# Kernel tuning notes

Hardware: AMD Instinct MI355X
Metric: run time of the kernel (lower is better)

## Reference

```python
import jax, jax.numpy as jnp
import numpy as np

B, L, D_IN, D_EDGE, H, D = 2, 384, 256, 128, 8, 32
SCALE = D ** (-0.5)


def setup_inputs() -> dict:
    key = jax.random.key(0)
    ks = jax.random.split(key, 12)
    hd = H * D
    s_in = D_IN ** -0.5
    s_e = D_EDGE ** -0.5
    return {
        "node_feat": jax.random.normal(ks[0], (B, L, D_IN), jnp.float32),
        "edge_feat": jax.random.normal(ks[1], (B, L, L, D_EDGE), jnp.float32),
        "edge_mask": (jax.random.uniform(ks[2], (B, L, L)) > 0.15).astype(jnp.float32),
        "Wq": jax.random.normal(ks[3], (D_IN, hd), jnp.float32) * s_in,
        "bq": jnp.zeros((hd,), jnp.float32),
        "Wk": jax.random.normal(ks[4], (D_IN, hd), jnp.float32) * s_in,
        "bk": jnp.zeros((hd,), jnp.float32),
        "Wv": jax.random.normal(ks[5], (D_IN, hd), jnp.float32) * s_in,
        "bv": jnp.zeros((hd,), jnp.float32),
        "We": jax.random.normal(ks[6], (D_EDGE, hd), jnp.float32) * s_e,
        "Wu": jax.random.normal(ks[7], (D_IN, hd), jnp.float32) * s_in,
        "bu": jnp.zeros((hd,), jnp.float32),
    }


def _split_heads(t):
    # (b, l, h*d) -> (b, h, l, d)
    b, l, _ = t.shape
    return t.reshape(b, l, H, D).transpose(0, 2, 1, 3)


def reference(node_feat, edge_feat, edge_mask, Wq, bq, Wk, bk, Wv, bv, We, Wu, bu):
    q = _split_heads(node_feat @ Wq + bq)
    k = _split_heads(node_feat @ Wk + bk)
    v = _split_heads(node_feat @ Wv + bv)
    # edge embedding: (b, i, j, h*d) -> (b, h, i, j, d)
    b, l = edge_feat.shape[0], edge_feat.shape[1]
    e = (edge_feat @ We).reshape(b, l, l, H, D).transpose(0, 3, 1, 2, 4)
    logit = jnp.einsum('bhid,bhjd->bhij', q, k)
    logit = logit + jnp.einsum('bhid,bhijd->bhij', q, e)
    att = logit * SCALE
    att = att + ((1.0 - edge_mask) * -1e9)[:, None, :, :]
    att = jax.nn.softmax(att, axis=-1)  # dropout is identity in eval / p=0
    updated = jnp.einsum('bhij,bhjd->bhid', att, v)
    updated = updated + jnp.einsum('bhij,bhijd->bhid', att, e)
    updated = updated.transpose(0, 2, 1, 3).reshape(b, l, H * D)
    return (node_feat @ Wu + bu) + updated
```

## Files before the change

### kernel.cpp

```cpp
#include <hip/hip_runtime.h>
#include <cstdint>

#define NB 2
#define LL 384
#define DIN 256
#define DE 128
#define NH 8
#define DH 32
#define HD 256
#define SCALE 0.17677669529663687f

typedef __attribute__((ext_vector_type(8))) short bf16x8;
typedef __attribute__((ext_vector_type(4))) float f32x4;

static __device__ __forceinline__ unsigned short f2bf(float f) {
    uint32_t u = __builtin_bit_cast(uint32_t, f);
    u += 0x7FFF + ((u >> 16) & 1);
    return (unsigned short)(u >> 16);
}
static __device__ __forceinline__ float bf2f(unsigned short u) {
    return __builtin_bit_cast(float, (uint32_t)u << 16);
}
static __device__ __forceinline__ float getf4(const float4& v, int k) {
    return k == 0 ? v.x : k == 1 ? v.y : k == 2 ? v.z : v.w;
}
static __device__ __forceinline__ bf16x8 pack8(const float4& a, const float4& b) {
    bf16x8 p;
    p[0]=(short)f2bf(a.x); p[1]=(short)f2bf(a.y); p[2]=(short)f2bf(a.z); p[3]=(short)f2bf(a.w);
    p[4]=(short)f2bf(b.x); p[5]=(short)f2bf(b.y); p[6]=(short)f2bf(b.z); p[7]=(short)f2bf(b.w);
    return p;
}

__global__ __launch_bounds__(128) void prep_we(const float* __restrict__ We,
                                               unsigned short* __restrict__ WeT) {
    const int n = blockIdx.x;
    const int k = threadIdx.x;
    WeT[n * DE + k] = f2bf(We[(size_t)k * HD + n]);
}

__global__ __launch_bounds__(256) void proj_kernel(
    const float* __restrict__ node,
    const float* __restrict__ Wq, const float* __restrict__ bq,
    const float* __restrict__ Wk, const float* __restrict__ bk,
    const float* __restrict__ Wv, const float* __restrict__ bv,
    const float* __restrict__ Wu, const float* __restrict__ bu,
    unsigned short* __restrict__ qb16, unsigned short* __restrict__ kb16,
    float* __restrict__ vb, float* __restrict__ ub)
{
    __shared__ __align__(16) float rows[4][DIN];
    const int t  = threadIdx.x;
    const int r0 = blockIdx.x * 4;

    #pragma unroll
    for (int r = 0; r < 4; ++r)
        rows[r][t] = node[(size_t)(r0 + r) * DIN + t];
    __syncthreads();

    float aq[4], ak[4], av[4], au[4];
    {
        const float vq = bq[t], vk = bk[t], vv = bv[t], vu = bu[t];
        #pragma unroll
        for (int r = 0; r < 4; ++r) { aq[r] = vq; ak[r] = vk; av[r] = vv; au[r] = vu; }
    }

    for (int f4 = 0; f4 < DIN / 4; ++f4) {
        float4 xv[4];
        #pragma unroll
        for (int r = 0; r < 4; ++r)
            xv[r] = *(const float4*)&rows[r][f4 * 4];
        #pragma unroll
        for (int k = 0; k < 4; ++k) {
            const int f = f4 * 4 + k;
            const float wq = Wq[(size_t)f * HD + t];
            const float wk = Wk[(size_t)f * HD + t];
            const float wv = Wv[(size_t)f * HD + t];
            const float wu = Wu[(size_t)f * HD + t];
            #pragma unroll
            for (int r = 0; r < 4; ++r) {
                const float x = getf4(xv[r], k);
                aq[r] += x * wq; ak[r] += x * wk; av[r] += x * wv; au[r] += x * wu;
            }
        }
    }

    #pragma unroll
    for (int r = 0; r < 4; ++r) {
        const size_t o = (size_t)(r0 + r) * HD + t;
        qb16[o] = f2bf(aq[r]); kb16[o] = f2bf(ak[r]);
        vb[o] = av[r]; ub[o] = au[r];
    }
}

__global__ __launch_bounds__(256) void vt_kernel(const float* __restrict__ vb,
                                                 unsigned short* __restrict__ vT) {
    __shared__ float tile[64][65];
    int blk = blockIdx.x;
    const int b  = blk / 24; blk %= 24;
    const int jt = blk / 4;
    const int ct = blk % 4;
    const int j0 = jt * 64, c0 = ct * 64;
    const int t  = threadIdx.x;
    const int c  = t & 63, j4 = t >> 6;
    #pragma unroll
    for (int rr = 0; rr < 16; ++rr) {
        const int j = j4 + 4 * rr;
        tile[j][c] = vb[(size_t)(b * LL + j0 + j) * HD + c0 + c];
    }
    __syncthreads();
    const int jj = t & 63, c4 = t >> 6;
    #pragma unroll
    for (int rr = 0; rr < 16; ++rr) {
        const int cc = c4 + 4 * rr;
        vT[(size_t)(b * HD + c0 + cc) * LL + j0 + jj] = f2bf(tile[jj][cc]);
    }
}

__global__ __launch_bounds__(256) void qk_kernel(
    const unsigned short* __restrict__ qb16, const unsigned short* __restrict__ kb16,
    const float* __restrict__ mask, float* __restrict__ logit_pre)
{
    int idx = blockIdx.x;
    const int jt = idx % 6; idx /= 6;
    const int it = idx % 6; idx /= 6;
    const int h  = idx % NH;
    const int b  = idx / NH;
    const int t    = threadIdx.x;
    const int lane = t & 63;
    const int w    = t >> 6;
    const int lid  = lane & 15;
    const int g    = lane >> 4;
    const int i0 = it * 64 + w * 16;
    const int j0 = jt * 64;

    const bf16x8 afr = *(const bf16x8*)&qb16[(size_t)(b * LL + i0 + lid) * HD + h * DH + g * 8];
    f32x4 acc[4];
    #pragma unroll
    for (int jj = 0; jj < 4; ++jj) {
        const bf16x8 bfrg = *(const bf16x8*)&kb16[(size_t)(b * LL + j0 + jj * 16 + lid) * HD + h * DH + g * 8];
        acc[jj] = __builtin_amdgcn_mfma_f32_16x16x32_bf16(afr, bfrg, (f32x4){0.f,0.f,0.f,0.f}, 0, 0, 0);
    }
    #pragma unroll
    for (int jj = 0; jj < 4; ++jj) {
        #pragma unroll
        for (int r = 0; r < 4; ++r) {
            const int i = i0 + 4 * g + r;
            const int j = j0 + jj * 16 + lid;
            const float lg = SCALE * acc[jj][r]
                           + (1.0f - mask[(size_t)(b * LL + i) * LL + j]) * -1e9f;
            logit_pre[((size_t)(b * NH + h) * LL + i) * LL + j] = lg;
        }
    }
}

__global__ __launch_bounds__(256) void qwe_kernel(
    const unsigned short* __restrict__ qb16, const unsigned short* __restrict__ WeT,
    unsigned short* __restrict__ qWe)
{
    const int bi = blockIdx.x;
    const int t  = threadIdx.x;
    const int h  = t >> 5;
    const int c0 = (t & 31) * 4;

    float qv[32];
    const unsigned short* qp = &qb16[(size_t)bi * HD + h * DH];
    #pragma unroll
    for (int d = 0; d < 32; ++d) qv[d] = bf2f(qp[d]);

    float acc0 = 0.f, acc1 = 0.f, acc2 = 0.f, acc3 = 0.f;
    #pragma unroll
    for (int d = 0; d < 32; ++d) {
        const ushort4 wt = *(const ushort4*)&WeT[(size_t)(h * DH + d) * DE + c0];
        acc0 += qv[d] * bf2f(wt.x); acc1 += qv[d] * bf2f(wt.y);
        acc2 += qv[d] * bf2f(wt.z); acc3 += qv[d] * bf2f(wt.w);
    }
    unsigned short* o = &qWe[(size_t)bi * (NH * DE) + h * DE + c0];
    o[0] = f2bf(SCALE * acc0); o[1] = f2bf(SCALE * acc1);
    o[2] = f2bf(SCALE * acc2); o[3] = f2bf(SCALE * acc3);
}

__global__ __launch_bounds__(512, 4) void fused_kernel(
    const float* __restrict__ edge,
    const unsigned short* __restrict__ qWe,
    const float* __restrict__ lpre,
    const unsigned short* __restrict__ vT,
    const float* __restrict__ We,
    const float* __restrict__ ub,
    float* __restrict__ out)
{
    __shared__ __align__(16) unsigned short p_lds[8 * 8 * 64];
    __shared__ float aEw[8 * NH * DE];
    __shared__ float avw[8 * HD];
    __shared__ float mlw[8][2][NH];
    __shared__ float aEm[NH * DE];

    const int t = threadIdx.x, lane = t & 63, w = t >> 6;
    const int lid = lane & 15, g = lane >> 4;
    const int bi = blockIdx.x, b = bi / LL, ii = bi % LL;
    const int j0w = w * 48;
    const int h8 = lid & 7;

    bf16x8 qfr[4];
    {
        const unsigned short* qwp = &qWe[(size_t)bi * (NH * DE) + h8 * DE];
        #pragma unroll
        for (int kt = 0; kt < 4; ++kt)
            qfr[kt] = *(const bf16x8*)&qwp[kt * 32 + g * 8];
    }

    f32x4 acc[3];
    #pragma unroll
    for (int mt = 0; mt < 3; ++mt) {
        acc[mt] = (f32x4){0.f, 0.f, 0.f, 0.f};
        const float* ef = edge + ((size_t)bi * LL + j0w + mt * 16 + lid) * DE;
        #pragma unroll
        for (int kt = 0; kt < 4; ++kt) {
            const float4 x0 = *(const float4*)&ef[kt * 32 + g * 8];
            const float4 x1 = *(const float4*)&ef[kt * 32 + g * 8 + 4];
            acc[mt] = __builtin_amdgcn_mfma_f32_16x16x32_bf16(pack8(x0, x1), qfr[kt], acc[mt], 0, 0, 0);
        }
    }

    const float* lrow = lpre + ((size_t)(b * NH + h8) * LL + ii) * LL;
    float lg[12];
    #pragma unroll
    for (int mt = 0; mt < 3; ++mt) {
        const float4 qk4 = *(const float4*)&lrow[j0w + mt * 16 + 4 * g];
        #pragma unroll
        for (int r = 0; r < 4; ++r)
            lg[mt * 4 + r] = (lid < 8) ? (acc[mt][r] + getf4(qk4, r)) : -3e38f;
    }

    float m = lg[0];
    #pragma unroll
    for (int k = 1; k < 12; ++k) m = fmaxf(m, lg[k]);
    m = fmaxf(m, __shfl_xor(m, 16));
    m = fmaxf(m, __shfl_xor(m, 32));
    float p[12], s = 0.f;
    #pragma unroll
    for (int k = 0; k < 12; ++k) { p[k] = __expf(lg[k] - m); s += p[k]; }
    s += __shfl_xor(s, 16); s += __shfl_xor(s, 32);
    if (lane < 8) { mlw[w][0][lane] = m; mlw[w][1][lane] = s; }

    unsigned short* pw = &p_lds[w * 512];
    if (lid < 8) {
        #pragma unroll
        for (int mt = 0; mt < 3; ++mt)
            #pragma unroll
            for (int r = 0; r < 4; ++r)
                pw[lid * 64 + mt * 16 + 4 * g + r] = f2bf(p[mt * 4 + r]);
    }
    ((unsigned int*)pw)[(lane >> 3) * 32 + 24 + (lane & 7)] = 0;

    bf16x8 pA[2];
    #pragma unroll
    for (int kt = 0; kt < 2; ++kt)
        pA[kt] = *(const bf16x8*)&pw[h8 * 64 + kt * 32 + g * 8];

    {
        float* aEp_w = &aEw[w * NH * DE];
        #pragma unroll
        for (int ct = 0; ct < 8; ++ct) {
            f32x4 aacc = (f32x4){0.f, 0.f, 0.f, 0.f};
            #pragma unroll
            for (int kt = 0; kt < 2; ++kt) {
                bf16x8 be;
                #pragma unroll
                for (int u = 0; u < 8; ++u) {
                    int jj = j0w + kt * 32 + g * 8 + u;
                    jj = jj > LL - 1 ? LL - 1 : jj;
                    be[u] = (short)f2bf(edge[((size_t)bi * LL + jj) * DE + ct * 16 + lid]);
                }
                aacc = __builtin_amdgcn_mfma_f32_16x16x32_bf16(pA[kt], be, aacc, 0, 0, 0);
            }
            if (g < 2) {
                #pragma unroll
                for (int r = 0; r < 4; ++r)
                    aEp_w[(4 * g + r) * DE + ct * 16 + lid] = aacc[r];
            }
        }
    }

    {
        float* av_w = &avw[w * HD];
        const unsigned short* vTb = vT + (size_t)b * HD * LL;
        #pragma unroll
        for (int nt = 0; nt < 16; ++nt) {
            f32x4 vacc = (f32x4){0.f, 0.f, 0.f, 0.f};
            #pragma unroll
            for (int kt = 0; kt < 2; ++kt) {
                const bf16x8 vv = *(const bf16x8*)&vTb[(size_t)(nt * 16 + lid) * LL + j0w + kt * 32 + g * 8];
                vacc = __builtin_amdgcn_mfma_f32_16x16x32_bf16(pA[kt], vv, vacc, 0, 0, 0);
            }
            const int hn = nt >> 1;
            if (g == (hn >> 2)) av_w[nt * 16 + lid] = vacc[hn & 3];
        }
    }

    __syncthreads();

    #pragma unroll
    for (int q = 0; q < 2; ++q) {
        const int idx = t + q * 512;
        const int h = idx >> 7, c = idx & 127;
        float M = mlw[0][0][h];
        #pragma unroll
        for (int w2 = 1; w2 < 8; ++w2) M = fmaxf(M, mlw[w2][0][h]);
        float L = 0.f, a = 0.f;
        #pragma unroll
        for (int w2 = 0; w2 < 8; ++w2) {
            const float f = __expf(mlw[w2][0][h] - M);
            L += f * mlw[w2][1][h];
            a += f * aEw[w2 * NH * DE + h * DE + c];
        }
        aEm[idx] = a / L;
    }
    __syncthreads();

    if (t < HD) {
        const int hd = t, h = hd >> 5;
        float M = mlw[0][0][h];
        #pragma unroll
        for (int w2 = 1; w2 < 8; ++w2) M = fmaxf(M, mlw[w2][0][h]);
        float L = 0.f, avv = 0.f;
        #pragma unroll
        for (int w2 = 0; w2 < 8; ++w2) {
            const float f = __expf(mlw[w2][0][h] - M);
            L += f * mlw[w2][1][h];
            avv += f * avw[w2 * HD + hd];
        }
        float o = ub[(size_t)bi * HD + hd] + avv / L;
        const float* sa = &aEm[h * DE];
        float a0 = 0.f, a1 = 0.f, a2 = 0.f, a3 = 0.f;
        #pragma unroll
        for (int c = 0; c < DE; c += 4) {
            a0 += sa[c]     * We[(size_t)(c)     * HD + hd];
            a1 += sa[c + 1] * We[(size_t)(c + 1) * HD + hd];
            a2 += sa[c + 2] * We[(size_t)(c + 2) * HD + hd];
            a3 += sa[c + 3] * We[(size_t)(c + 3) * HD + hd];
        }
        out[(size_t)bi * HD + hd] = o + ((a0 + a1) + (a2 + a3));
    }
}

extern "C" void kernel_launch(void* const* d_in, const int* in_sizes, int n_in,
                              void* d_out, int out_size, void* d_ws, size_t ws_size,
                              hipStream_t stream) {
    const float* node = (const float*)d_in[0];
    const float* edge = (const float*)d_in[1];
    const float* mask = (const float*)d_in[2];
    const float* Wq   = (const float*)d_in[3];
    const float* bq   = (const float*)d_in[4];
    const float* Wk   = (const float*)d_in[5];
    const float* bk   = (const float*)d_in[6];
    const float* Wv   = (const float*)d_in[7];
    const float* bv   = (const float*)d_in[8];
    const float* We   = (const float*)d_in[9];
    const float* Wu   = (const float*)d_in[10];
    const float* bu   = (const float*)d_in[11];
    float* out = (float*)d_out;

    const size_t rowsz = (size_t)NB * LL * HD;
    const size_t lsz   = (size_t)NB * NH * LL * LL;
    float* ws   = (float*)d_ws;
    float* vb   = ws;
    float* ubuf = vb + rowsz;
    float* lpre = ubuf + rowsz;
    unsigned short* us   = (unsigned short*)(lpre + lsz);
    unsigned short* WeT  = us;
    unsigned short* qb16 = WeT + (size_t)HD * DE;
    unsigned short* kb16 = qb16 + rowsz;
    unsigned short* vT   = kb16 + rowsz;
    unsigned short* qWeB = vT + rowsz;

    hipLaunchKernelGGL(prep_we, dim3(HD), dim3(DE), 0, stream, We, WeT);
    hipLaunchKernelGGL(proj_kernel, dim3(NB * LL / 4), dim3(256), 0, stream,
                       node, Wq, bq, Wk, bk, Wv, bv, Wu, bu, qb16, kb16, vb, ubuf);
    hipLaunchKernelGGL(vt_kernel, dim3(NB * (LL / 64) * (HD / 64)), dim3(256), 0, stream,
                       vb, vT);
    hipLaunchKernelGGL(qk_kernel, dim3(NB * NH * (LL / 64) * (LL / 64)), dim3(256), 0, stream,
                       qb16, kb16, mask, lpre);
    hipLaunchKernelGGL(qwe_kernel, dim3(NB * LL), dim3(256), 0, stream,
                       qb16, WeT, qWeB);
    hipLaunchKernelGGL(fused_kernel, dim3(NB * LL), dim3(512), 0, stream,
                       edge, qWeB, lpre, vT, We, ubuf, out);
}
```

Before: 114.4 us.

## Stage edge row in LDS as bf16 and do full-row softmax before aggregation

The fused kernel now converts the edge row to bf16 once and stores it in an XOR-swizzled LDS tile. The second pass (attention times edge) reads that tile instead of re-reading edge from global memory with strided scalar loads. Softmax normalisation now finishes across all warps before aggregation, so each warp computes full-length MFMA reductions over all 384 keys for its slice of output channels, and the per-warp partial merge is gone. It also issues edge and logit loads early to overlap latency. In exchange, LDS use grows to about 100KB per block and launch bounds drop to one block per SM, which lowers occupancy and adds a barrier.

```diff
diff --git a/kernel.cpp b/kernel.cpp
--- a/kernel.cpp
+++ b/kernel.cpp
@@ -9,6 +9,7 @@
 #define DH 32
 #define HD 256
 #define SCALE 0.17677669529663687f
+#define PBS 400
 
 typedef __attribute__((ext_vector_type(8))) short bf16x8;
 typedef __attribute__((ext_vector_type(4))) float f32x4;
@@ -178,7 +179,7 @@
     o[2] = f2bf(SCALE * acc2); o[3] = f2bf(SCALE * acc3);
 }
 
-__global__ __launch_bounds__(512, 4) void fused_kernel(
+__global__ __launch_bounds__(512, 1) void fused2_kernel(
     const float* __restrict__ edge,
     const unsigned short* __restrict__ qWe,
     const float* __restrict__ lpre,
@@ -187,11 +188,11 @@
     const float* __restrict__ ub,
     float* __restrict__ out)
 {
-    __shared__ __align__(16) unsigned short p_lds[8 * 8 * 64];
-    __shared__ float aEw[8 * NH * DE];
-    __shared__ float avw[8 * HD];
+    __shared__ __align__(16) unsigned short Es[LL * DE];
+    __shared__ __align__(16) unsigned short pb[NH * PBS];
     __shared__ float mlw[8][2][NH];
     __shared__ float aEm[NH * DE];
+    __shared__ float avs[HD];
 
     const int t = threadIdx.x, lane = t & 63, w = t >> 6;
     const int lid = lane & 15, g = lane >> 4;
@@ -199,6 +200,22 @@
     const int j0w = w * 48;
     const int h8 = lid & 7;
 
+    float4 eL[3][4][2];
+    #pragma unroll
+    for (int mt = 0; mt < 3; ++mt) {
+        const float* ef = edge + ((size_t)bi * LL + j0w + mt * 16 + lid) * DE;
+        #pragma unroll
+        for (int kt = 0; kt < 4; ++kt) {
+            eL[mt][kt][0] = *(const float4*)&ef[kt * 32 + g * 8];
+            eL[mt][kt][1] = *(const float4*)&ef[kt * 32 + g * 8 + 4];
+        }
+    }
+    float4 qk4[3];
+    const float* lrow = lpre + ((size_t)(b * NH + h8) * LL + ii) * LL;
+    #pragma unroll
+    for (int mt = 0; mt < 3; ++mt)
+        qk4[mt] = *(const float4*)&lrow[j0w + mt * 16 + 4 * g];
+
     bf16x8 qfr[4];
     {
         const unsigned short* qwp = &qWe[(size_t)bi * (NH * DE) + h8 * DE];
@@ -211,24 +228,21 @@
     #pragma unroll
     for (int mt = 0; mt < 3; ++mt) {
         acc[mt] = (f32x4){0.f, 0.f, 0.f, 0.f};
-        const float* ef = edge + ((size_t)bi * LL + j0w + mt * 16 + lid) * DE;
+        const int j = j0w + mt * 16 + lid;
         #pragma unroll
         for (int kt = 0; kt < 4; ++kt) {
-            const float4 x0 = *(const float4*)&ef[kt * 32 + g * 8];
-            const float4 x1 = *(const float4*)&ef[kt * 32 + g * 8 + 4];
-            acc[mt] = __builtin_amdgcn_mfma_f32_16x16x32_bf16(pack8(x0, x1), qfr[kt], acc[mt], 0, 0, 0);
-        }
-    }
-
-    const float* lrow = lpre + ((size_t)(b * NH + h8) * LL + ii) * LL;
+            const bf16x8 pk = pack8(eL[mt][kt][0], eL[mt][kt][1]);
+            *(bf16x8*)&Es[j * DE + (((kt * 4 + g) ^ (j & 15)) << 3)] = pk;
+            acc[mt] = __builtin_amdgcn_mfma_f32_16x16x32_bf16(pk, qfr[kt], acc[mt], 0, 0, 0);
+        }
+    }
+
     float lg[12];
     #pragma unroll
-    for (int mt = 0; mt < 3; ++mt) {
-        const float4 qk4 = *(const float4*)&lrow[j0w + mt * 16 + 4 * g];
+    for (int mt = 0; mt < 3; ++mt)
         #pragma unroll
         for (int r = 0; r < 4; ++r)
-            lg[mt * 4 + r] = (lid < 8) ? (acc[mt][r] + getf4(qk4, r)) : -3e38f;
-    }
+            lg[mt * 4 + r] = (lid < 8) ? (acc[mt][r] + getf4(qk4[mt], r)) : -3e38f;
 
     float m = lg[0];
     #pragma unroll
@@ -241,94 +255,78 @@
     s += __shfl_xor(s, 16); s += __shfl_xor(s, 32);
     if (lane < 8) { mlw[w][0][lane] = m; mlw[w][1][lane] = s; }
 
-    unsigned short* pw = &p_lds[w * 512];
-    if (lid < 8) {
-        #pragma unroll
-        for (int mt = 0; mt < 3; ++mt)
-            #pragma unroll
-            for (int r = 0; r < 4; ++r)
-                pw[lid * 64 + mt * 16 + 4 * g + r] = f2bf(p[mt * 4 + r]);
-    }
-    ((unsigned int*)pw)[(lane >> 3) * 32 + 24 + (lane & 7)] = 0;
-
-    bf16x8 pA[2];
-    #pragma unroll
-    for (int kt = 0; kt < 2; ++kt)
-        pA[kt] = *(const bf16x8*)&pw[h8 * 64 + kt * 32 + g * 8];
-
-    {
-        float* aEp_w = &aEw[w * NH * DE];
-        #pragma unroll
-        for (int ct = 0; ct < 8; ++ct) {
-            f32x4 aacc = (f32x4){0.f, 0.f, 0.f, 0.f};
-            #pragma unroll
-            for (int kt = 0; kt < 2; ++kt) {
-                bf16x8 be;
-                #pragma unroll
-                for (int u = 0; u < 8; ++u) {
-                    int jj = j0w + kt * 32 + g * 8 + u;
-                    jj = jj > LL - 1 ? LL - 1 : jj;
-                    be[u] = (short)f2bf(edge[((size_t)bi * LL + jj) * DE + ct * 16 + lid]);
-                }
-                aacc = __builtin_amdgcn_mfma_f32_16x16x32_bf16(pA[kt], be, aacc, 0, 0, 0);
-            }
-            if (g < 2) {
+    __syncthreads();
+
+    {
+        float M = mlw[0][0][h8];
+        #pragma unroll
+        for (int w2 = 1; w2 < 8; ++w2) M = fmaxf(M, mlw[w2][0][h8]);
+        float Lsum = 0.f;
+        #pragma unroll
+        for (int w2 = 0; w2 < 8; ++w2)
+            Lsum += __expf(mlw[w2][0][h8] - M) * mlw[w2][1][h8];
+        const float f = __expf(m - M) / Lsum;
+        if (lid < 8) {
+            #pragma unroll
+            for (int mt = 0; mt < 3; ++mt)
                 #pragma unroll
                 for (int r = 0; r < 4; ++r)
-                    aEp_w[(4 * g + r) * DE + ct * 16 + lid] = aacc[r];
+                    pb[h8 * PBS + j0w + mt * 16 + 4 * g + r] = f2bf(p[mt * 4 + r] * f);
+        }
+    }
+
+    __syncthreads();
+
+    bf16x8 pA[12];
+    #pragma unroll
+    for (int kt = 0; kt < 12; ++kt)
+        pA[kt] = *(const bf16x8*)&pb[h8 * PBS + kt * 32 + g * 8];
+
+    {
+        const int cE = 16 * w + lid, chE = cE >> 3, ceE = cE & 7;
+        f32x4 accE = (f32x4){0.f, 0.f, 0.f, 0.f};
+        #pragma unroll
+        for (int kt = 0; kt < 12; ++kt) {
+            bf16x8 be;
+            #pragma unroll
+            for (int u = 0; u < 8; ++u) {
+                const int k = kt * 32 + g * 8 + u;
+                be[u] = (short)Es[k * DE + ((chE ^ (k & 15)) << 3) + ceE];
             }
-        }
-    }
-
-    {
-        float* av_w = &avw[w * HD];
+            accE = __builtin_amdgcn_mfma_f32_16x16x32_bf16(pA[kt], be, accE, 0, 0, 0);
+        }
+        if (g < 2) {
+            #pragma unroll
+            for (int r = 0; r < 4; ++r)
+                aEm[(4 * g + r) * DE + cE] = accE[r];
+        }
+    }
+
+    {
         const unsigned short* vTb = vT + (size_t)b * HD * LL;
         #pragma unroll
-        for (int nt = 0; nt < 16; ++nt) {
-            f32x4 vacc = (f32x4){0.f, 0.f, 0.f, 0.f};
-            #pragma unroll
-            for (int kt = 0; kt < 2; ++kt) {
-                const bf16x8 vv = *(const bf16x8*)&vTb[(size_t)(nt * 16 + lid) * LL + j0w + kt * 32 + g * 8];
-                vacc = __builtin_amdgcn_mfma_f32_16x16x32_bf16(pA[kt], vv, vacc, 0, 0, 0);
+        for (int mm = 0; mm < 2; ++mm) {
+            const int hd = (2 * w + mm) * 16 + lid;
+            const unsigned short* vr = &vTb[(size_t)hd * LL];
+            f32x4 accV = (f32x4){0.f, 0.f, 0.f, 0.f};
+            #pragma unroll
+            for (int kt = 0; kt < 12; ++kt) {
+                const bf16x8 vv = *(const bf16x8*)&vr[kt * 32 + g * 8];
+                accV = __builtin_amdgcn_mfma_f32_16x16x32_bf16(pA[kt], vv, accV, 0, 0, 0);
             }
-            const int hn = nt >> 1;
-            if (g == (hn >> 2)) av_w[nt * 16 + lid] = vacc[hn & 3];
-        }
-    }
-
-    __syncthreads();
-
-    #pragma unroll
-    for (int q = 0; q < 2; ++q) {
-        const int idx = t + q * 512;
-        const int h = idx >> 7, c = idx & 127;
-        float M = mlw[0][0][h];
-        #pragma unroll
-        for (int w2 = 1; w2 < 8; ++w2) M = fmaxf(M, mlw[w2][0][h]);
-        float L = 0.f, a = 0.f;
-        #pragma unroll
-        for (int w2 = 0; w2 < 8; ++w2) {
-            const float f = __expf(mlw[w2][0][h] - M);
-            L += f * mlw[w2][1][h];
-            a += f * aEw[w2 * NH * DE + h * DE + c];
-        }
-        aEm[idx] = a / L;
-    }
+            if ((w >> 2) == g) {
+                const int r = w & 3;
+                const float val = r == 0 ? accV[0] : r == 1 ? accV[1] : r == 2 ? accV[2] : accV[3];
+                avs[hd] = val;
+            }
+        }
+    }
+
     __syncthreads();
 
     if (t < HD) {
         const int hd = t, h = hd >> 5;
-        float M = mlw[0][0][h];
-        #pragma unroll
-        for (int w2 = 1; w2 < 8; ++w2) M = fmaxf(M, mlw[w2][0][h]);
-        float L = 0.f, avv = 0.f;
-        #pragma unroll
-        for (int w2 = 0; w2 < 8; ++w2) {
-            const float f = __expf(mlw[w2][0][h] - M);
-            L += f * mlw[w2][1][h];
-            avv += f * avw[w2 * HD + hd];
-        }
-        float o = ub[(size_t)bi * HD + hd] + avv / L;
+        float o = ub[(size_t)bi * HD + hd] + avs[hd];
         const float* sa = &aEm[h * DE];
         float a0 = 0.f, a1 = 0.f, a2 = 0.f, a3 = 0.f;
         #pragma unroll
@@ -381,6 +379,6 @@
                        qb16, kb16, mask, lpre);
     hipLaunchKernelGGL(qwe_kernel, dim3(NB * LL), dim3(256), 0, stream,
                        qb16, WeT, qWeB);
-    hipLaunchKernelGGL(fused_kernel, dim3(NB * LL), dim3(512), 0, stream,
+    hipLaunchKernelGGL(fused2_kernel, dim3(NB * LL), dim3(512), 0, stream,
                        edge, qWeB, lpre, vT, We, ubuf, out);
 }
```

After: 109.5 us. -4.3%, faster.
